# Kernel tuning notes

Measured on AMD Instinct MI355X. Metric: run time of the kernel, lower is better.

The kernel has to match this reference:

```python
import jax, jax.numpy as jnp
import numpy as np

H = 256
VOCAB = 32000
B = 128
T = 2048


def setup_inputs() -> dict:
    key = jax.random.key(0)
    ks = jax.random.split(key, 14)
    s = 0.05
    return {
        "tokens": jax.random.randint(ks[0], (B, 1), 0, VOCAB),
        "hidden": jax.random.normal(ks[1], (1, B, H), jnp.float32),
        "encoder_outputs": jax.random.normal(ks[2], (T, B, H), jnp.float32),
        "emb_table": jax.random.normal(ks[3], (VOCAB + 1, H), jnp.float32) * s,
        "attn_W": jax.random.normal(ks[4], (1, 2 * H), jnp.float32) * s,
        "attn_b": jax.random.normal(ks[5], (1,), jnp.float32) * s,
        "comb_W": jax.random.normal(ks[6], (H, 2 * H), jnp.float32) * s,
        "comb_b": jax.random.normal(ks[7], (H,), jnp.float32) * s,
        "gru_Wih": jax.random.normal(ks[8], (3 * H, H), jnp.float32) * s,
        "gru_Whh": jax.random.normal(ks[9], (3 * H, H), jnp.float32) * s,
        "gru_bih": jax.random.normal(ks[10], (3 * H,), jnp.float32) * s,
        "gru_bhh": jax.random.normal(ks[11], (3 * H,), jnp.float32) * s,
        "out_W": jax.random.normal(ks[12], (VOCAB, H), jnp.float32) * s,
        "out_b": jax.random.normal(ks[13], (VOCAB,), jnp.float32) * s,
    }


def reference(tokens, hidden, encoder_outputs, emb_table, attn_W, attn_b,
              comb_W, comb_b, gru_Wih, gru_Whh, gru_bih, gru_bhh, out_W, out_b):
    h = hidden.shape[-1]
    # Embedding lookup: [B,1] -> [B,1,H] -> [1,B,H]
    emb = jnp.transpose(emb_table[tokens], (1, 0, 2))
    # Additive attention: Linear([hidden; enc_t]) -> scalar score per position.
    # attn_W splits into hidden part (first H cols) and encoder part (last H).
    W_h, W_e = attn_W[:, :h], attn_W[:, h:]          # [1,H] each
    scores = (jnp.einsum('tbh,oh->tbo', encoder_outputs, W_e)
              + jnp.einsum('lbh,oh->lbo', hidden, W_h)  # broadcast over T
              + attn_b)                                  # [T,B,1]
    attn_w = jax.nn.softmax(scores, axis=0)              # softmax over time
    # Context: weighted sum over time -> [1,B,H]
    ctx = jnp.einsum('tbo,tbh->obh', attn_w, encoder_outputs)
    # Combine embedded input with context, relu
    x = jnp.concatenate([emb, ctx], axis=2)              # [1,B,2H]
    x = jax.nn.relu(jnp.einsum('lbk,hk->lbh', x, comb_W) + comb_b)  # [1,B,H]
    # Single GRU step (PyTorch gate ordering: r, z, n)
    gx = x[0] @ gru_Wih.T + gru_bih                      # [B,3H]
    gh = hidden[0] @ gru_Whh.T + gru_bhh                 # [B,3H]
    r = jax.nn.sigmoid(gx[:, :h] + gh[:, :h])
    z = jax.nn.sigmoid(gx[:, h:2 * h] + gh[:, h:2 * h])
    n = jnp.tanh(gx[:, 2 * h:] + r * gh[:, 2 * h:])
    h_new = ((1.0 - z) * n + z * hidden[0])[None]        # [1,B,H]
    # Output projection + log_softmax over vocab
    logits = jnp.einsum('lbh,vh->lbv', h_new, out_W) + out_b
    logp = jax.nn.log_softmax(logits, axis=2)            # [1,B,V]
    return (logp, h_new, jnp.transpose(attn_w, (1, 0, 2)), ctx)
```

## Files before the change

kernel.cpp:

```cpp
#include <hip/hip_runtime.h>
#include <cstddef>

constexpr int H  = 256;
constexpr int Bb = 128;
constexpr int T  = 2048;
constexpr int V  = 32000;
constexpr int SPLITS = 16;
constexpr int TC = T / SPLITS;
constexpr int NPART = SPLITS * 4;
constexpr int LSE_SPLIT = 4;
constexpr int VS = V / LSE_SPLIT;

typedef __attribute__((ext_vector_type(8))) short short8;
typedef __attribute__((ext_vector_type(4))) float f32x4;

__device__ __forceinline__ unsigned short bf1(float a) {
  unsigned u = __builtin_bit_cast(unsigned, a);
  return (unsigned short)((u + 0x7fffu + ((u >> 16) & 1u)) >> 16);
}
__device__ __forceinline__ unsigned bfpack2(float a, float b) {
  unsigned ua = __builtin_bit_cast(unsigned, a);
  unsigned ub = __builtin_bit_cast(unsigned, b);
  ua = (ua + 0x7fffu + ((ua >> 16) & 1u)) >> 16;
  ub = (ub + 0x7fffu + ((ub >> 16) & 1u)) & 0xffff0000u;
  return ua | ub;
}

__global__ __launch_bounds__(256) void k_attn(
    const float* __restrict__ enc, const float* __restrict__ hidden,
    const float* __restrict__ attn_W, const float* __restrict__ attn_b,
    float* __restrict__ scores, float* __restrict__ ctx_part) {
  const int b = blockIdx.y, chunk = blockIdx.x;
  const int tid = threadIdx.x, lane = tid & 63, wave = tid >> 6;

  const float4 we = *(const float4*)(attn_W + H + lane * 4);
  const float4 wh = *(const float4*)(attn_W + lane * 4);
  const float4 hv = *(const float4*)(hidden + (size_t)b * H + lane * 4);

  float hb = fmaf(wh.x, hv.x, fmaf(wh.y, hv.y, fmaf(wh.z, hv.z, wh.w * hv.w)));
  #pragma unroll
  for (int off = 1; off < 64; off <<= 1) hb += __shfl_xor(hb, off);
  hb += attn_b[0];

  const int t0 = chunk * TC + wave * 32;
  const float* base = enc + (size_t)t0 * (Bb * H) + (size_t)b * H + lane * 4;

  float4 acc = {0.f, 0.f, 0.f, 0.f};
  for (int i = 0; i < 32; i += 4) {
    float4 e0 = *(const float4*)(base + (size_t)(i + 0) * (Bb * H));
    float4 e1 = *(const float4*)(base + (size_t)(i + 1) * (Bb * H));
    float4 e2 = *(const float4*)(base + (size_t)(i + 2) * (Bb * H));
    float4 e3 = *(const float4*)(base + (size_t)(i + 3) * (Bb * H));

    float p0 = fmaf(e0.x, we.x, fmaf(e0.y, we.y, fmaf(e0.z, we.z, e0.w * we.w)));
    float p1 = fmaf(e1.x, we.x, fmaf(e1.y, we.y, fmaf(e1.z, we.z, e1.w * we.w)));
    float p2 = fmaf(e2.x, we.x, fmaf(e2.y, we.y, fmaf(e2.z, we.z, e2.w * we.w)));
    float p3 = fmaf(e3.x, we.x, fmaf(e3.y, we.y, fmaf(e3.z, we.z, e3.w * we.w)));
    #pragma unroll
    for (int off = 1; off < 64; off <<= 1) {
      p0 += __shfl_xor(p0, off);
      p1 += __shfl_xor(p1, off);
      p2 += __shfl_xor(p2, off);
      p3 += __shfl_xor(p3, off);
    }
    float s0 = p0 + hb, s1 = p1 + hb, s2 = p2 + hb, s3 = p3 + hb;
    float w0 = __expf(s0), w1 = __expf(s1), w2 = __expf(s2), w3 = __expf(s3);

    acc.x = fmaf(w0, e0.x, fmaf(w1, e1.x, fmaf(w2, e2.x, fmaf(w3, e3.x, acc.x))));
    acc.y = fmaf(w0, e0.y, fmaf(w1, e1.y, fmaf(w2, e2.y, fmaf(w3, e3.y, acc.y))));
    acc.z = fmaf(w0, e0.z, fmaf(w1, e1.z, fmaf(w2, e2.z, fmaf(w3, e3.z, acc.z))));
    acc.w = fmaf(w0, e0.w, fmaf(w1, e1.w, fmaf(w2, e2.w, fmaf(w3, e3.w, acc.w))));

    if (lane == 0) {
      float4 sv = {s0, s1, s2, s3};
      *(float4*)(scores + (size_t)b * T + t0 + i) = sv;
    }
  }
  float* cp = ctx_part + ((size_t)b * NPART + chunk * 4 + wave) * H + lane * 4;
  *(float4*)cp = acc;
}

__global__ __launch_bounds__(256) void k_softmax_ctx(
    const float* __restrict__ scores, const float* __restrict__ ctx_part,
    float* __restrict__ attn_o, float* __restrict__ ctx_o) {
  const int b = blockIdx.x, tid = threadIdx.x;
  const int lane = tid & 63, wave = tid >> 6;
  __shared__ float red[4];
  __shared__ float m_sh, l_sh;

  const float* sb = scores + (size_t)b * T;
  float s[8];
  #pragma unroll
  for (int q = 0; q < 8; q++) s[q] = sb[tid + 256 * q];

  float mx = s[0];
  #pragma unroll
  for (int q = 1; q < 8; q++) mx = fmaxf(mx, s[q]);
  #pragma unroll
  for (int off = 1; off < 64; off <<= 1) mx = fmaxf(mx, __shfl_xor(mx, off));
  if (lane == 0) red[wave] = mx;
  __syncthreads();
  if (tid == 0) m_sh = fmaxf(fmaxf(red[0], red[1]), fmaxf(red[2], red[3]));
  __syncthreads();
  const float m = m_sh;

  float w[8];
  float ps = 0.f;
  #pragma unroll
  for (int q = 0; q < 8; q++) { w[q] = __expf(s[q] - m); ps += w[q]; }
  #pragma unroll
  for (int off = 1; off < 64; off <<= 1) ps += __shfl_xor(ps, off);
  __syncthreads();
  if (lane == 0) red[wave] = ps;
  __syncthreads();
  if (tid == 0) l_sh = red[0] + red[1] + red[2] + red[3];
  __syncthreads();
  const float inv = 1.f / l_sh;

  #pragma unroll
  for (int q = 0; q < 8; q++) attn_o[(size_t)b * T + tid + 256 * q] = w[q] * inv;

  float c = 0.f;
  for (int si = 0; si < NPART; si++)
    c += ctx_part[((size_t)b * NPART + si) * H + tid];
  ctx_o[(size_t)b * H + tid] = c * __expf(-m) * inv;
}

__global__ __launch_bounds__(256) void k_comb_gru(
    const int* __restrict__ tokens, const float* __restrict__ hidden,
    const float* __restrict__ emb_table,
    const float* __restrict__ comb_W, const float* __restrict__ comb_b,
    const float* __restrict__ Wih, const float* __restrict__ Whh,
    const float* __restrict__ bih, const float* __restrict__ bhh,
    const float* __restrict__ ctx_o, float* __restrict__ hnew,
    unsigned short* __restrict__ hnewb) {
  const int b = blockIdx.x, tid = threadIdx.x;
  __shared__ __align__(16) float x2[2 * H];
  __shared__ __align__(16) float hid[H];
  __shared__ __align__(16) float xs[H];

  const int tok = tokens[b];
  x2[tid]     = emb_table[(size_t)tok * H + tid];
  x2[H + tid] = ctx_o[(size_t)b * H + tid];
  hid[tid]    = hidden[(size_t)b * H + tid];
  __syncthreads();

  {
    const float4* wr = (const float4*)(comb_W + (size_t)tid * (2 * H));
    const float4* xr = (const float4*)x2;
    float a = 0.f;
    #pragma unroll 8
    for (int k = 0; k < (2 * H) / 4; k++) {
      float4 w = wr[k], x = xr[k];
      a += w.x * x.x + w.y * x.y + w.z * x.z + w.w * x.w;
    }
    a += comb_b[tid];
    xs[tid] = fmaxf(a, 0.f);
  }
  __syncthreads();

  auto dot256 = [](const float* __restrict__ row, const float* __restrict__ v) -> float {
    const float4* r4 = (const float4*)row;
    const float4* v4 = (const float4*)v;
    float a = 0.f;
    #pragma unroll 8
    for (int k = 0; k < H / 4; k++) {
      float4 w = r4[k], x = v4[k];
      a += w.x * x.x + w.y * x.y + w.z * x.z + w.w * x.w;
    }
    return a;
  };

  float gxr = dot256(Wih + (size_t)tid * H,           xs) + bih[tid];
  float gxz = dot256(Wih + (size_t)(tid + H) * H,     xs) + bih[tid + H];
  float gxn = dot256(Wih + (size_t)(tid + 2 * H) * H, xs) + bih[tid + 2 * H];
  float ghr = dot256(Whh + (size_t)tid * H,           hid) + bhh[tid];
  float ghz = dot256(Whh + (size_t)(tid + H) * H,     hid) + bhh[tid + H];
  float ghn = dot256(Whh + (size_t)(tid + 2 * H) * H, hid) + bhh[tid + 2 * H];

  float r = 1.f / (1.f + __expf(-(gxr + ghr)));
  float z = 1.f / (1.f + __expf(-(gxz + ghz)));
  float n = tanhf(gxn + r * ghn);
  float hv = (1.f - z) * n + z * hid[tid];
  hnew[(size_t)b * H + tid] = hv;
  hnewb[(size_t)b * H + tid] = bf1(hv);
}

constexpr int LSTR = 72;
__global__ __launch_bounds__(256) void k_logits(
    const unsigned short* __restrict__ hnewb, const float* __restrict__ out_W,
    const float* __restrict__ out_b, float* __restrict__ logits) {
  const int tid = threadIdx.x;
  const int lane = tid & 63, wave = tid >> 6;
  const int v0 = blockIdx.x * 128;
  const int r16 = lane & 15, quad = lane >> 4;

  __shared__ __align__(16) short lA[128 * LSTR];
  __shared__ __align__(16) short lB[128 * LSTR];

  f32x4 acc[8][2];
  #pragma unroll
  for (int mt = 0; mt < 8; mt++) {
    acc[mt][0] = (f32x4){0.f, 0.f, 0.f, 0.f};
    acc[mt][1] = (f32x4){0.f, 0.f, 0.f, 0.f};
  }

  for (int k0 = 0; k0 < H; k0 += 64) {
    #pragma unroll
    for (int q = 0; q < 4; q++) {
      int idx = q * 256 + tid;
      int row = idx >> 3, c8 = idx & 7;
      f32x4 v = *(const f32x4*)(hnewb + (size_t)row * H + k0 + c8 * 8);
      *(f32x4*)(&lA[row * LSTR + c8 * 8]) = v;
    }
    #pragma unroll
    for (int q = 0; q < 8; q++) {
      int idx = q * 256 + tid;
      int row = idx >> 4, c4 = idx & 15;
      f32x4 wv = *(const f32x4*)(out_W + (size_t)(v0 + row) * H + k0 + c4 * 4);
      uint2 p;
      p.x = bfpack2(wv.x, wv.y);
      p.y = bfpack2(wv.z, wv.w);
      *(uint2*)(&lB[row * LSTR + c4 * 4]) = p;
    }
    __syncthreads();
    #pragma unroll
    for (int ks = 0; ks < 2; ks++) {
      short8 bf[2];
      #pragma unroll
      for (int nt = 0; nt < 2; nt++) {
        int row = wave * 32 + nt * 16 + r16;
        bf[nt] = *(const short8*)(&lB[row * LSTR + ks * 32 + quad * 8]);
      }
      #pragma unroll
      for (int mt = 0; mt < 8; mt++) {
        short8 af = *(const short8*)(&lA[(mt * 16 + r16) * LSTR + ks * 32 + quad * 8]);
        acc[mt][0] = __builtin_amdgcn_mfma_f32_16x16x32_bf16(af, bf[0], acc[mt][0], 0, 0, 0);
        acc[mt][1] = __builtin_amdgcn_mfma_f32_16x16x32_bf16(af, bf[1], acc[mt][1], 0, 0, 0);
      }
    }
    __syncthreads();
  }

  #pragma unroll
  for (int nt = 0; nt < 2; nt++) {
    int col = v0 + wave * 32 + nt * 16 + r16;
    float bias = out_b[col];
    #pragma unroll
    for (int mt = 0; mt < 8; mt++) {
      int brow = mt * 16 + quad * 4;
      #pragma unroll
      for (int r = 0; r < 4; r++)
        logits[(size_t)(brow + r) * V + col] = acc[mt][nt][r] + bias;
    }
  }
}

__global__ __launch_bounds__(256) void k_lse(
    const float* __restrict__ logits, float2* __restrict__ lse_part) {
  const int b = blockIdx.x, s = blockIdx.y, tid = threadIdx.x;
  const int lane = tid & 63, wave = tid >> 6;
  const float4* base = (const float4*)(logits + (size_t)b * V + (size_t)s * VS);

  float4 m4 = {-1e30f, -1e30f, -1e30f, -1e30f};
  float4 l4 = {0.f, 0.f, 0.f, 0.f};
  for (int i = tid; i < VS / 4; i += 256) {
    float4 x = base[i];
    float nm;
    nm = fmaxf(m4.x, x.x); l4.x = l4.x * __expf(m4.x - nm) + __expf(x.x - nm); m4.x = nm;
    nm = fmaxf(m4.y, x.y); l4.y = l4.y * __expf(m4.y - nm) + __expf(x.y - nm); m4.y = nm;
    nm = fmaxf(m4.z, x.z); l4.z = l4.z * __expf(m4.z - nm) + __expf(x.z - nm); m4.z = nm;
    nm = fmaxf(m4.w, x.w); l4.w = l4.w * __expf(m4.w - nm) + __expf(x.w - nm); m4.w = nm;
  }
  float m = fmaxf(fmaxf(m4.x, m4.y), fmaxf(m4.z, m4.w));
  float l = l4.x * __expf(m4.x - m) + l4.y * __expf(m4.y - m) +
            l4.z * __expf(m4.z - m) + l4.w * __expf(m4.w - m);
  #pragma unroll
  for (int off = 1; off < 64; off <<= 1) {
    float mo = __shfl_xor(m, off), lo = __shfl_xor(l, off);
    float nm = fmaxf(m, mo);
    l = l * __expf(m - nm) + lo * __expf(mo - nm);
    m = nm;
  }
  __shared__ float sm[4], sl[4];
  if (lane == 0) { sm[wave] = m; sl[wave] = l; }
  __syncthreads();
  if (tid == 0) {
    float M = sm[0], L = sl[0];
    #pragma unroll
    for (int w2 = 1; w2 < 4; w2++) {
      float nm = fmaxf(M, sm[w2]);
      L = L * __expf(M - nm) + sl[w2] * __expf(sm[w2] - nm);
      M = nm;
    }
    lse_part[b * LSE_SPLIT + s] = make_float2(M, L);
  }
}

__global__ __launch_bounds__(256) void k_sub(
    float* __restrict__ logits, const float2* __restrict__ lse_part) {
  const int b = blockIdx.y;
  const int i = blockIdx.x * 256 + threadIdx.x;
  float2 p0 = lse_part[b * 4 + 0], p1 = lse_part[b * 4 + 1];
  float2 p2 = lse_part[b * 4 + 2], p3 = lse_part[b * 4 + 3];
  float M = fmaxf(fmaxf(p0.x, p1.x), fmaxf(p2.x, p3.x));
  float L = p0.y * __expf(p0.x - M) + p1.y * __expf(p1.x - M) +
            p2.y * __expf(p2.x - M) + p3.y * __expf(p3.x - M);
  float lse = M + logf(L);
  if (i < V / 4) {
    float4* p = (float4*)(logits + (size_t)b * V) + i;
    float4 x = *p;
    x.x -= lse; x.y -= lse; x.z -= lse; x.w -= lse;
    *p = x;
  }
}

extern "C" void kernel_launch(void* const* d_in, const int* in_sizes, int n_in,
                              void* d_out, int out_size, void* d_ws, size_t ws_size,
                              hipStream_t stream) {
  const int*   tokens = (const int*)d_in[0];
  const float* hidden = (const float*)d_in[1];
  const float* enc    = (const float*)d_in[2];
  const float* emb    = (const float*)d_in[3];
  const float* attn_W = (const float*)d_in[4];
  const float* attn_b = (const float*)d_in[5];
  const float* comb_W = (const float*)d_in[6];
  const float* comb_b = (const float*)d_in[7];
  const float* Wih    = (const float*)d_in[8];
  const float* Whh    = (const float*)d_in[9];
  const float* bih    = (const float*)d_in[10];
  const float* bhh    = (const float*)d_in[11];
  const float* out_W  = (const float*)d_in[12];
  const float* out_b  = (const float*)d_in[13];

  float* out    = (float*)d_out;
  float* logp   = out;
  float* hnew   = out + (size_t)Bb * V;
  float* attn_o = hnew + (size_t)Bb * H;
  float* ctx_o  = attn_o + (size_t)Bb * T;

  float* ws       = (float*)d_ws;
  float* scores   = ws;
  float* ctx_part = ws + (size_t)Bb * T;
  float2* lse_part = (float2*)(ctx_part + (size_t)Bb * NPART * H);
  unsigned short* hnewb = (unsigned short*)(lse_part + Bb * LSE_SPLIT);

  k_attn<<<dim3(SPLITS, Bb), 256, 0, stream>>>(enc, hidden, attn_W, attn_b, scores, ctx_part);
  k_softmax_ctx<<<dim3(Bb), 256, 0, stream>>>(scores, ctx_part, attn_o, ctx_o);
  k_comb_gru<<<dim3(Bb), 256, 0, stream>>>(tokens, hidden, emb, comb_W, comb_b,
                                           Wih, Whh, bih, bhh, ctx_o, hnew, hnewb);
  k_logits<<<dim3(V / 128), 256, 0, stream>>>(hnewb, out_W, out_b, logp);
  k_lse<<<dim3(Bb, LSE_SPLIT), 256, 0, stream>>>(logp, lse_part);
  k_sub<<<dim3(V / 1024 + 1, Bb), 256, 0, stream>>>(logp, lse_part);
}
```

Baseline: 508.5 us.

## Fuse softmax into GRU kernel and log-softmax into logits via grid barrier

Merges the attention softmax/context kernel into the combine+GRU kernel, passing the context through registers. The logits kernel now computes per-block partial max/sum-exp from its accumulators, uses a software grid barrier (atomic counter) to combine them into per-row log-sum-exp, and writes final log-probabilities directly. This drops the separate LSE and subtract kernels and the extra read-modify-write of the 16MB logits buffer. It relies on all 250 blocks being co-resident for the spin barrier, and the barrier counter is reset by the previous kernel.

```diff
diff --git a/kernel.cpp b/kernel.cpp
--- a/kernel.cpp
+++ b/kernel.cpp
@@ -8,8 +8,7 @@
 constexpr int SPLITS = 16;
 constexpr int TC = T / SPLITS;
 constexpr int NPART = SPLITS * 4;
-constexpr int LSE_SPLIT = 4;
-constexpr int VS = V / LSE_SPLIT;
+constexpr int NVB = V / 128;
 
 typedef __attribute__((ext_vector_type(8))) short short8;
 typedef __attribute__((ext_vector_type(4))) float f32x4;
@@ -26,6 +25,17 @@
   return ua | ub;
 }
 
+__device__ __forceinline__ void gsync(int* bar, int target) {
+  __syncthreads();
+  if (threadIdx.x == 0) {
+    __threadfence();
+    __hip_atomic_fetch_add(bar, 1, __ATOMIC_RELEASE, __HIP_MEMORY_SCOPE_AGENT);
+    while (__hip_atomic_load(bar, __ATOMIC_ACQUIRE, __HIP_MEMORY_SCOPE_AGENT) < target)
+      __builtin_amdgcn_s_sleep(8);
+  }
+  __syncthreads();
+}
+
 __global__ __launch_bounds__(256) void k_attn(
     const float* __restrict__ enc, const float* __restrict__ hidden,
     const float* __restrict__ attn_W, const float* __restrict__ attn_b,
@@ -80,68 +90,67 @@
   *(float4*)cp = acc;
 }
 
-__global__ __launch_bounds__(256) void k_softmax_ctx(
+__global__ __launch_bounds__(256) void k_smx_gru(
     const float* __restrict__ scores, const float* __restrict__ ctx_part,
-    float* __restrict__ attn_o, float* __restrict__ ctx_o) {
-  const int b = blockIdx.x, tid = threadIdx.x;
-  const int lane = tid & 63, wave = tid >> 6;
-  __shared__ float red[4];
-  __shared__ float m_sh, l_sh;
-
-  const float* sb = scores + (size_t)b * T;
-  float s[8];
-  #pragma unroll
-  for (int q = 0; q < 8; q++) s[q] = sb[tid + 256 * q];
-
-  float mx = s[0];
-  #pragma unroll
-  for (int q = 1; q < 8; q++) mx = fmaxf(mx, s[q]);
-  #pragma unroll
-  for (int off = 1; off < 64; off <<= 1) mx = fmaxf(mx, __shfl_xor(mx, off));
-  if (lane == 0) red[wave] = mx;
-  __syncthreads();
-  if (tid == 0) m_sh = fmaxf(fmaxf(red[0], red[1]), fmaxf(red[2], red[3]));
-  __syncthreads();
-  const float m = m_sh;
-
-  float w[8];
-  float ps = 0.f;
-  #pragma unroll
-  for (int q = 0; q < 8; q++) { w[q] = __expf(s[q] - m); ps += w[q]; }
-  #pragma unroll
-  for (int off = 1; off < 64; off <<= 1) ps += __shfl_xor(ps, off);
-  __syncthreads();
-  if (lane == 0) red[wave] = ps;
-  __syncthreads();
-  if (tid == 0) l_sh = red[0] + red[1] + red[2] + red[3];
-  __syncthreads();
-  const float inv = 1.f / l_sh;
-
-  #pragma unroll
-  for (int q = 0; q < 8; q++) attn_o[(size_t)b * T + tid + 256 * q] = w[q] * inv;
-
-  float c = 0.f;
-  for (int si = 0; si < NPART; si++)
-    c += ctx_part[((size_t)b * NPART + si) * H + tid];
-  ctx_o[(size_t)b * H + tid] = c * __expf(-m) * inv;
-}
-
-__global__ __launch_bounds__(256) void k_comb_gru(
     const int* __restrict__ tokens, const float* __restrict__ hidden,
     const float* __restrict__ emb_table,
     const float* __restrict__ comb_W, const float* __restrict__ comb_b,
     const float* __restrict__ Wih, const float* __restrict__ Whh,
     const float* __restrict__ bih, const float* __restrict__ bhh,
-    const float* __restrict__ ctx_o, float* __restrict__ hnew,
-    unsigned short* __restrict__ hnewb) {
+    float* __restrict__ attn_o, float* __restrict__ ctx_o,
+    float* __restrict__ hnew, unsigned short* __restrict__ hnewb,
+    int* __restrict__ bar) {
   const int b = blockIdx.x, tid = threadIdx.x;
+  const int lane = tid & 63, wave = tid >> 6;
+  __shared__ float red[4];
+  __shared__ float m_sh, l_sh;
   __shared__ __align__(16) float x2[2 * H];
   __shared__ __align__(16) float hid[H];
   __shared__ __align__(16) float xs[H];
 
+  if (b == 0 && tid == 0) bar[0] = 0;
+
+  const float* sb = scores + (size_t)b * T;
+  float s[8];
+  #pragma unroll
+  for (int q = 0; q < 8; q++) s[q] = sb[tid + 256 * q];
+
+  float mx = s[0];
+  #pragma unroll
+  for (int q = 1; q < 8; q++) mx = fmaxf(mx, s[q]);
+  #pragma unroll
+  for (int off = 1; off < 64; off <<= 1) mx = fmaxf(mx, __shfl_xor(mx, off));
+  if (lane == 0) red[wave] = mx;
+  __syncthreads();
+  if (tid == 0) m_sh = fmaxf(fmaxf(red[0], red[1]), fmaxf(red[2], red[3]));
+  __syncthreads();
+  const float m = m_sh;
+
+  float w[8];
+  float ps = 0.f;
+  #pragma unroll
+  for (int q = 0; q < 8; q++) { w[q] = __expf(s[q] - m); ps += w[q]; }
+  #pragma unroll
+  for (int off = 1; off < 64; off <<= 1) ps += __shfl_xor(ps, off);
+  __syncthreads();
+  if (lane == 0) red[wave] = ps;
+  __syncthreads();
+  if (tid == 0) l_sh = red[0] + red[1] + red[2] + red[3];
+  __syncthreads();
+  const float inv = 1.f / l_sh;
+
+  #pragma unroll
+  for (int q = 0; q < 8; q++) attn_o[(size_t)b * T + tid + 256 * q] = w[q] * inv;
+
+  float c = 0.f;
+  for (int si = 0; si < NPART; si++)
+    c += ctx_part[((size_t)b * NPART + si) * H + tid];
+  const float ctxv = c * __expf(-m) * inv;
+  ctx_o[(size_t)b * H + tid] = ctxv;
+
   const int tok = tokens[b];
   x2[tid]     = emb_table[(size_t)tok * H + tid];
-  x2[H + tid] = ctx_o[(size_t)b * H + tid];
+  x2[H + tid] = ctxv;
   hid[tid]    = hidden[(size_t)b * H + tid];
   __syncthreads();
 
@@ -151,8 +160,8 @@
     float a = 0.f;
     #pragma unroll 8
     for (int k = 0; k < (2 * H) / 4; k++) {
-      float4 w = wr[k], x = xr[k];
-      a += w.x * x.x + w.y * x.y + w.z * x.z + w.w * x.w;
+      float4 ww = wr[k], x = xr[k];
+      a += ww.x * x.x + ww.y * x.y + ww.z * x.z + ww.w * x.w;
     }
     a += comb_b[tid];
     xs[tid] = fmaxf(a, 0.f);
@@ -165,8 +174,8 @@
     float a = 0.f;
     #pragma unroll 8
     for (int k = 0; k < H / 4; k++) {
-      float4 w = r4[k], x = v4[k];
-      a += w.x * x.x + w.y * x.y + w.z * x.z + w.w * x.w;
+      float4 ww = r4[k], x = v4[k];
+      a += ww.x * x.x + ww.y * x.y + ww.z * x.z + ww.w * x.w;
     }
     return a;
   };
@@ -187,16 +196,21 @@
 }
 
 constexpr int LSTR = 72;
-__global__ __launch_bounds__(256) void k_logits(
+__global__ __launch_bounds__(256) void k_logits_fused(
     const unsigned short* __restrict__ hnewb, const float* __restrict__ out_W,
-    const float* __restrict__ out_b, float* __restrict__ logits) {
+    const float* __restrict__ out_b, float* __restrict__ logp,
+    float2* __restrict__ part, float* __restrict__ lse_g,
+    int* __restrict__ bar) {
   const int tid = threadIdx.x;
   const int lane = tid & 63, wave = tid >> 6;
-  const int v0 = blockIdx.x * 128;
+  const int blk = blockIdx.x;
+  const int v0 = blk * 128;
   const int r16 = lane & 15, quad = lane >> 4;
 
   __shared__ __align__(16) short lA[128 * LSTR];
   __shared__ __align__(16) short lB[128 * LSTR];
+  __shared__ float2 lred[4 * 128];
+  __shared__ float lse_s[128];
 
   f32x4 acc[8][2];
   #pragma unroll
@@ -242,76 +256,94 @@
     __syncthreads();
   }
 
+  const float bias0 = out_b[v0 + wave * 32 + r16];
+  const float bias1 = out_b[v0 + wave * 32 + 16 + r16];
+
+  #pragma unroll
+  for (int mt = 0; mt < 8; mt++) {
+    float pm[4], pl[4];
+    #pragma unroll
+    for (int r = 0; r < 4; r++) {
+      float x0 = acc[mt][0][r] + bias0;
+      float x1 = acc[mt][1][r] + bias1;
+      float mm = fmaxf(x0, x1);
+      pm[r] = mm;
+      pl[r] = __expf(x0 - mm) + __expf(x1 - mm);
+    }
+    #pragma unroll
+    for (int off = 1; off < 16; off <<= 1) {
+      #pragma unroll
+      for (int r = 0; r < 4; r++) {
+        float mo = __shfl_xor(pm[r], off), lo = __shfl_xor(pl[r], off);
+        float nm = fmaxf(pm[r], mo);
+        pl[r] = pl[r] * __expf(pm[r] - nm) + lo * __expf(mo - nm);
+        pm[r] = nm;
+      }
+    }
+    if (r16 == 0) {
+      #pragma unroll
+      for (int r = 0; r < 4; r++)
+        lred[wave * 128 + mt * 16 + quad * 4 + r] = make_float2(pm[r], pl[r]);
+    }
+  }
+  __syncthreads();
+  if (tid < 128) {
+    float2 p = lred[tid];
+    #pragma unroll
+    for (int w2 = 1; w2 < 4; w2++) {
+      float2 q = lred[w2 * 128 + tid];
+      float nm = fmaxf(p.x, q.x);
+      p.y = p.y * __expf(p.x - nm) + q.y * __expf(q.x - nm);
+      p.x = nm;
+    }
+    part[(size_t)tid * NVB + blk] = p;
+  }
+
+  gsync(bar, NVB);
+
+  if (blk < 128) {
+    float pm = -1e30f, pl = 0.f;
+    if (tid < NVB) {
+      float2 p = part[(size_t)blk * NVB + tid];
+      pm = p.x; pl = p.y;
+    }
+    #pragma unroll
+    for (int off = 1; off < 64; off <<= 1) {
+      float mo = __shfl_xor(pm, off), lo = __shfl_xor(pl, off);
+      float nm = fmaxf(pm, mo);
+      pl = pl * __expf(pm - nm) + lo * __expf(mo - nm);
+      pm = nm;
+    }
+    if (lane == 0) lred[wave] = make_float2(pm, pl);
+    __syncthreads();
+    if (tid == 0) {
+      float2 p = lred[0];
+      #pragma unroll
+      for (int w2 = 1; w2 < 4; w2++) {
+        float2 q = lred[w2];
+        float nm = fmaxf(p.x, q.x);
+        p.y = p.y * __expf(p.x - nm) + q.y * __expf(q.x - nm);
+        p.x = nm;
+      }
+      lse_g[blk] = p.x + logf(p.y);
+    }
+  }
+
+  gsync(bar, 2 * NVB);
+
+  if (tid < 128) lse_s[tid] = lse_g[tid];
+  __syncthreads();
   #pragma unroll
   for (int nt = 0; nt < 2; nt++) {
     int col = v0 + wave * 32 + nt * 16 + r16;
-    float bias = out_b[col];
+    float bias = nt ? bias1 : bias0;
     #pragma unroll
     for (int mt = 0; mt < 8; mt++) {
       int brow = mt * 16 + quad * 4;
       #pragma unroll
       for (int r = 0; r < 4; r++)
-        logits[(size_t)(brow + r) * V + col] = acc[mt][nt][r] + bias;
-    }
-  }
-}
-
-__global__ __launch_bounds__(256) void k_lse(
-    const float* __restrict__ logits, float2* __restrict__ lse_part) {
-  const int b = blockIdx.x, s = blockIdx.y, tid = threadIdx.x;
-  const int lane = tid & 63, wave = tid >> 6;
-  const float4* base = (const float4*)(logits + (size_t)b * V + (size_t)s * VS);
-
-  float4 m4 = {-1e30f, -1e30f, -1e30f, -1e30f};
-  float4 l4 = {0.f, 0.f, 0.f, 0.f};
-  for (int i = tid; i < VS / 4; i += 256) {
-    float4 x = base[i];
-    float nm;
-    nm = fmaxf(m4.x, x.x); l4.x = l4.x * __expf(m4.x - nm) + __expf(x.x - nm); m4.x = nm;
-    nm = fmaxf(m4.y, x.y); l4.y = l4.y * __expf(m4.y - nm) + __expf(x.y - nm); m4.y = nm;
-    nm = fmaxf(m4.z, x.z); l4.z = l4.z * __expf(m4.z - nm) + __expf(x.z - nm); m4.z = nm;
-    nm = fmaxf(m4.w, x.w); l4.w = l4.w * __expf(m4.w - nm) + __expf(x.w - nm); m4.w = nm;
-  }
-  float m = fmaxf(fmaxf(m4.x, m4.y), fmaxf(m4.z, m4.w));
-  float l = l4.x * __expf(m4.x - m) + l4.y * __expf(m4.y - m) +
-            l4.z * __expf(m4.z - m) + l4.w * __expf(m4.w - m);
-  #pragma unroll
-  for (int off = 1; off < 64; off <<= 1) {
-    float mo = __shfl_xor(m, off), lo = __shfl_xor(l, off);
-    float nm = fmaxf(m, mo);
-    l = l * __expf(m - nm) + lo * __expf(mo - nm);
-    m = nm;
-  }
-  __shared__ float sm[4], sl[4];
-  if (lane == 0) { sm[wave] = m; sl[wave] = l; }
-  __syncthreads();
-  if (tid == 0) {
-    float M = sm[0], L = sl[0];
-    #pragma unroll
-    for (int w2 = 1; w2 < 4; w2++) {
-      float nm = fmaxf(M, sm[w2]);
-      L = L * __expf(M - nm) + sl[w2] * __expf(sm[w2] - nm);
-      M = nm;
-    }
-    lse_part[b * LSE_SPLIT + s] = make_float2(M, L);
-  }
-}
-
-__global__ __launch_bounds__(256) void k_sub(
-    float* __restrict__ logits, const float2* __restrict__ lse_part) {
-  const int b = blockIdx.y;
-  const int i = blockIdx.x * 256 + threadIdx.x;
-  float2 p0 = lse_part[b * 4 + 0], p1 = lse_part[b * 4 + 1];
-  float2 p2 = lse_part[b * 4 + 2], p3 = lse_part[b * 4 + 3];
-  float M = fmaxf(fmaxf(p0.x, p1.x), fmaxf(p2.x, p3.x));
-  float L = p0.y * __expf(p0.x - M) + p1.y * __expf(p1.x - M) +
-            p2.y * __expf(p2.x - M) + p3.y * __expf(p3.x - M);
-  float lse = M + logf(L);
-  if (i < V / 4) {
-    float4* p = (float4*)(logits + (size_t)b * V) + i;
-    float4 x = *p;
-    x.x -= lse; x.y -= lse; x.z -= lse; x.w -= lse;
-    *p = x;
+        logp[(size_t)(brow + r) * V + col] = acc[mt][nt][r] + bias - lse_s[brow + r];
+    }
   }
 }
 
@@ -342,14 +374,15 @@
   float* ws       = (float*)d_ws;
   float* scores   = ws;
   float* ctx_part = ws + (size_t)Bb * T;
-  float2* lse_part = (float2*)(ctx_part + (size_t)Bb * NPART * H);
-  unsigned short* hnewb = (unsigned short*)(lse_part + Bb * LSE_SPLIT);
+  float2* part    = (float2*)(ctx_part + (size_t)Bb * NPART * H);
+  float* lse_g    = (float*)(part + (size_t)Bb * NVB);
+  unsigned short* hnewb = (unsigned short*)(lse_g + Bb);
+  int* bar        = (int*)(hnewb + (size_t)Bb * H);
 
   k_attn<<<dim3(SPLITS, Bb), 256, 0, stream>>>(enc, hidden, attn_W, attn_b, scores, ctx_part);
-  k_softmax_ctx<<<dim3(Bb), 256, 0, stream>>>(scores, ctx_part, attn_o, ctx_o);
-  k_comb_gru<<<dim3(Bb), 256, 0, stream>>>(tokens, hidden, emb, comb_W, comb_b,
-                                           Wih, Whh, bih, bhh, ctx_o, hnew, hnewb);
-  k_logits<<<dim3(V / 128), 256, 0, stream>>>(hnewb, out_W, out_b, logp);
-  k_lse<<<dim3(Bb, LSE_SPLIT), 256, 0, stream>>>(logp, lse_part);
-  k_sub<<<dim3(V / 1024 + 1, Bb), 256, 0, stream>>>(logp, lse_part);
-}
+  k_smx_gru<<<dim3(Bb), 256, 0, stream>>>(scores, ctx_part, tokens, hidden, emb,
+                                          comb_W, comb_b, Wih, Whh, bih, bhh,
+                                          attn_o, ctx_o, hnew, hnewb, bar);
+  k_logits_fused<<<dim3(NVB), 256, 0, stream>>>(hnewb, out_W, out_b, logp,
+                                                part, lse_g, bar);
+}
```

New measurement: 538.1 us. 1.06x slower.
